# Optimization experiments

Measured on AMD Instinct MI355X. Metric: run time of the kernel, lower is better.

## Reference

```python
import jax, jax.numpy as jnp
import numpy as np

SEQ_LEN = 1024
BATCH = 256
HIDDEN = 100
OUT = 1

L_FILTER = [-0.0106, 0.0329, 0.0308, -0.187, -0.028, 0.6309, 0.7148, 0.2304]
H_FILTER = [-0.2304, 0.7148, -0.6309, -0.028, 0.187, 0.0308, -0.0329, -0.0106]


def _create_W(P, is_l, rng):
    filt = L_FILTER if is_l else H_FILTER
    eps = np.min(np.abs(filt))
    W = rng.standard_normal((P, P)) * 0.1 * eps
    for i in range(P):
        for k, j in enumerate(range(i, min(i + len(filt), P))):
            W[i, j] = filt[k]
    return jnp.asarray(W, dtype=jnp.float32)


def setup_inputs() -> dict:
    key = jax.random.key(0)
    ks = jax.random.split(key, 16)
    rng = np.random.default_rng(0)
    T, H = SEQ_LEN, HIDDEN
    s = 1.0 / np.sqrt(H)

    def lstm_params(k):
        k1, k2, k3 = jax.random.split(k, 3)
        Wih = jax.random.uniform(k1, (4 * H, 1), jnp.float32, -s, s)
        Whh = jax.random.uniform(k2, (4 * H, H), jnp.float32, -s, s)
        b = jax.random.uniform(k3, (4 * H,), jnp.float32, -s, s)
        return Wih, Whh, b

    Wih1, Whh1, b1 = lstm_params(ks[0])
    Wih2, Whh2, b2 = lstm_params(ks[1])
    Wih3, Whh3, b3 = lstm_params(ks[2])
    return {
        "x": jax.random.normal(ks[3], (BATCH, T, 1), jnp.float32),
        "W1H": _create_W(T, False, rng),
        "b1H": jax.random.uniform(ks[4], (T,), jnp.float32, -1 / np.sqrt(T), 1 / np.sqrt(T)),
        "W1L": _create_W(T, True, rng),
        "b1L": jax.random.uniform(ks[5], (T,), jnp.float32, -1 / np.sqrt(T), 1 / np.sqrt(T)),
        "W2H": _create_W(T // 2, False, rng),
        "b2H": jax.random.uniform(ks[6], (T // 2,), jnp.float32, -1 / np.sqrt(T // 2), 1 / np.sqrt(T // 2)),
        "W2L": _create_W(T // 2, True, rng),
        "b2L": jax.random.uniform(ks[7], (T // 2,), jnp.float32, -1 / np.sqrt(T // 2), 1 / np.sqrt(T // 2)),
        "Wih1": Wih1, "Whh1": Whh1, "b1": b1,
        "Wih2": Wih2, "Whh2": Whh2, "b2": b2,
        "Wih3": Wih3, "Whh3": Whh3, "b3": b3,
        "Wout": jax.random.uniform(ks[8], (OUT, H), jnp.float32, -s, s),
        "bout": jax.random.uniform(ks[9], (OUT,), jnp.float32, -s, s),
    }


def _avgpool2(x):  # [B, L] -> [B, L//2], AvgPool1d(kernel=2, stride=2)
    B, L = x.shape
    return x.reshape(B, L // 2, 2).mean(-1)


def _lstm(x, Wih, Whh, b):
    # x: [B, T, 1]; torch LSTM gate order i, f, g, o; h0 = c0 = 0
    H = Whh.shape[1]
    gx = jnp.einsum('bti,gi->btg', x, Wih) + b  # [B, T, 4H]

    def step(carry, g):
        h, c = carry
        z = g + h @ Whh.T
        i, f, gg, o = jnp.split(z, 4, axis=-1)
        c = jax.nn.sigmoid(f) * c + jax.nn.sigmoid(i) * jnp.tanh(gg)
        h = jax.nn.sigmoid(o) * jnp.tanh(c)
        return (h, c), h

    B = x.shape[0]
    h0 = jnp.zeros((B, H), x.dtype)
    _, hs = jax.lax.scan(step, (h0, h0), jnp.swapaxes(gx, 0, 1))
    return jnp.swapaxes(hs, 0, 1)  # [B, T, H]


def reference(x, W1H, b1H, W1L, b1L, W2H, b2H, W2L, b2L,
              Wih1, Whh1, b1, Wih2, Whh2, b2, Wih3, Whh3, b3, Wout, bout):
    inp = x[:, :, -1]  # [B, T]
    ah1 = jax.nn.sigmoid(inp @ W1H.T + b1H)
    al1 = jax.nn.sigmoid(inp @ W1L.T + b1L)
    xh1 = _avgpool2(ah1)  # [B, T/2]
    xl1 = _avgpool2(al1)  # [B, T/2]
    ah2 = jax.nn.sigmoid(xl1 @ W2H.T + b2H)
    al2 = jax.nn.sigmoid(xl1 @ W2L.T + b2L)
    xh2 = _avgpool2(ah2)  # [B, T/4]
    xl2 = _avgpool2(al2)  # [B, T/4]
    s1 = _lstm(xh1[..., None], Wih1, Whh1, b1)
    s2 = _lstm(xh2[..., None], Wih2, Whh2, b2)
    s3 = _lstm(xl2[..., None], Wih3, Whh3, b3)
    cat = jnp.concatenate([s1, s2, s3], axis=1)  # [B, T, H]
    out = cat @ Wout.T + bout  # [B, T, OUT]
    return out[:, -1, :]
```

## Files before the change

### kernel.cpp

```cpp
#include <hip/hip_runtime.h>
#include <math.h>

typedef __bf16 bf16x8 __attribute__((ext_vector_type(8)));
typedef _Float16 f16x8 __attribute__((ext_vector_type(8)));
typedef _Float16 f16x4 __attribute__((ext_vector_type(4)));
typedef float f32x4 __attribute__((ext_vector_type(4)));

#define LOG2E 1.44269504f
#define TWOL2E 2.88539008f

__device__ __forceinline__ unsigned short f2bf(float f) {
  unsigned int u = __builtin_bit_cast(unsigned int, f);
  u += 0x7fffu + ((u >> 16) & 1u);
  return (unsigned short)(u >> 16);
}
__device__ __forceinline__ unsigned int pack2bf(float a, float b) {
  return (unsigned int)f2bf(a) | ((unsigned int)f2bf(b) << 16);
}

#define GK_PAD2 72
template <int WFP32, int XFP32, int DO_PREP, int NXB>
__global__ __launch_bounds__(256) void gemm_mfma_sig_pool(
    const void* __restrict__ Wv, const float* __restrict__ bias,
    const void* __restrict__ Xv, void* __restrict__ Y,
    int K, int Np, int out_bf16,
    const float* __restrict__ Whh, const float* __restrict__ b3,
    _Float16* __restrict__ P) {
  if (DO_PREP && blockIdx.x == NXB) {
    const int base = blockIdx.y * 256 + threadIdx.x;
    for (int idx = base; idx < 400 * 16; idx += 4096) {
      const int row = idx >> 4, ch = idx & 15;
      const int hid = row >> 2, gate = row & 3;
      const int src = gate * 100 + hid;
      const float s = (gate == 2) ? TWOL2E : LOG2E;
      f16x8 v;
#pragma unroll
      for (int j = 0; j < 8; j++) {
        const int k = ch * 8 + j;
        float f = 0.f;
        if (k < 100) f = Whh[(size_t)src * 100 + k] * s;
        v[j] = (_Float16)f;
      }
      *(f16x8*)&P[(size_t)row * 128 + ch * 8] = v;
    }
    return;
  }

  __shared__ unsigned short Wt[64][GK_PAD2];
  __shared__ unsigned short Xt[16][GK_PAD2];
  const int tid = threadIdx.x;
  const int i_base = blockIdx.x * 64;
  const int b_base = blockIdx.y * 16;
  const int srow = tid >> 2, sseg = tid & 3;
  const int xr = tid >> 4, xs = tid & 15;
  const int wv = tid >> 6, lane = tid & 63;
  const int L15 = lane & 15, q = lane >> 4;

  const float* Wf = (const float*)Wv;
  const float* Xf = (const float*)Xv;
  const unsigned short* Wh = (const unsigned short*)Wv;
  const unsigned short* Xh = (const unsigned short*)Xv;

  float4 wf[2][4];
  uint4 wh[2][2];
  float4 xf[2];
  uint2 xh2[2];

#define LOADW(S, KO)                                                          \
  do {                                                                        \
    if (WFP32) {                                                              \
      _Pragma("unroll") for (int j = 0; j < 4; j++)                           \
          wf[S][j] = *(const float4*)&Wf[(size_t)(i_base + srow) * K + (KO) + \
                                         sseg * 16 + 4 * j];                  \
    } else {                                                                  \
      _Pragma("unroll") for (int j = 0; j < 2; j++)                           \
          wh[S][j] = *(const uint4*)&Wh[(size_t)(i_base + srow) * K + (KO) +  \
                                        sseg * 16 + 8 * j];                   \
    }                                                                         \
  } while (0)

#define LOADX(S, KO)                                                          \
  do {                                                                        \
    if (XFP32) {                                                              \
      xf[S] = *(const float4*)&Xf[(size_t)(b_base + xr) * K + (KO) + xs * 4]; \
    } else {                                                                  \
      xh2[S] = *(const uint2*)&Xh[(size_t)(b_base + xr) * K + (KO) + xs * 4]; \
    }                                                                         \
  } while (0)

#define STAGEW(S)                                                             \
  do {                                                                        \
    if (WFP32) {                                                              \
      uint4 p0 = {pack2bf(wf[S][0].x, wf[S][0].y),                            \
                  pack2bf(wf[S][0].z, wf[S][0].w),                            \
                  pack2bf(wf[S][1].x, wf[S][1].y),                            \
                  pack2bf(wf[S][1].z, wf[S][1].w)};                           \
      uint4 p1 = {pack2bf(wf[S][2].x, wf[S][2].y),                            \
                  pack2bf(wf[S][2].z, wf[S][2].w),                            \
                  pack2bf(wf[S][3].x, wf[S][3].y),                            \
                  pack2bf(wf[S][3].z, wf[S][3].w)};                           \
      *(uint4*)&Wt[srow][sseg * 16] = p0;                                     \
      *(uint4*)&Wt[srow][sseg * 16 + 8] = p1;                                 \
    } else {                                                                  \
      *(uint4*)&Wt[srow][sseg * 16] = wh[S][0];                               \
      *(uint4*)&Wt[srow][sseg * 16 + 8] = wh[S][1];                           \
    }                                                                         \
  } while (0)

#define STAGEX(S)                                                             \
  do {                                                                        \
    if (XFP32) {                                                              \
      uint2 p = {pack2bf(xf[S].x, xf[S].y), pack2bf(xf[S].z, xf[S].w)};       \
      *(uint2*)&Xt[xr][xs * 4] = p;                                           \
    } else {                                                                  \
      *(uint2*)&Xt[xr][xs * 4] = xh2[S];                                      \
    }                                                                         \
  } while (0)

#define DOMFMA                                                                \
  do {                                                                        \
    _Pragma("unroll") for (int kt = 0; kt < 2; kt++) {                        \
      bf16x8 a = *(const bf16x8*)&Wt[wv * 16 + L15][kt * 32 + q * 8];         \
      bf16x8 b = *(const bf16x8*)&Xt[L15][kt * 32 + q * 8];                   \
      acc = __builtin_amdgcn_mfma_f32_16x16x32_bf16(a, b, acc, 0, 0, 0);      \
    }                                                                         \
  } while (0)

  f32x4 acc = {};
  LOADW(0, 0);
  LOADX(0, 0);
  for (int k0 = 0; k0 < K; k0 += 128) {
    LOADW(1, k0 + 64);
    LOADX(1, k0 + 64);
    STAGEW(0);
    STAGEX(0);
    __syncthreads();
    DOMFMA;
    __syncthreads();
    if (k0 + 128 < K) {
      LOADW(0, k0 + 128);
      LOADX(0, k0 + 128);
    }
    STAGEW(1);
    STAGEX(1);
    __syncthreads();
    DOMFMA;
    __syncthreads();
  }
#undef LOADW
#undef LOADX
#undef STAGEW
#undef STAGEX
#undef DOMFMA

  {
    const int nrow = i_base + 16 * wv + q * 4;
    const float bi0 = bias[nrow], bi1 = bias[nrow + 1];
    const float bi2 = bias[nrow + 2], bi3 = bias[nrow + 3];
    const int b = b_base + L15;
    const float a0 = __builtin_amdgcn_rcpf(1.f + __expf(-(acc[0] + bi0)));
    const float a1 = __builtin_amdgcn_rcpf(1.f + __expf(-(acc[1] + bi1)));
    const float a2 = __builtin_amdgcn_rcpf(1.f + __expf(-(acc[2] + bi2)));
    const float a3 = __builtin_amdgcn_rcpf(1.f + __expf(-(acc[3] + bi3)));
    const float p0 = 0.5f * (a0 + a1), p1 = 0.5f * (a2 + a3);
    const int pidx = nrow >> 1;
    if (out_bf16) {
      *(unsigned int*)&((unsigned short*)Y)[(size_t)b * Np + pidx] = pack2bf(p0, p1);
    } else {
      *(float2*)&((float*)Y)[(size_t)b * Np + pidx] = make_float2(p0, p1);
    }
  }
}

#define TSTEPS 256

__device__ __forceinline__ float qb0(float x) {
  return __builtin_bit_cast(float, __builtin_amdgcn_mov_dpp(__builtin_bit_cast(int, x), 0x00, 0xf, 0xf, true));
}
__device__ __forceinline__ float qb1(float x) {
  return __builtin_bit_cast(float, __builtin_amdgcn_mov_dpp(__builtin_bit_cast(int, x), 0x55, 0xf, 0xf, true));
}
__device__ __forceinline__ float qb2(float x) {
  return __builtin_bit_cast(float, __builtin_amdgcn_mov_dpp(__builtin_bit_cast(int, x), 0xAA, 0xf, 0xf, true));
}
__device__ __forceinline__ float qb3(float x) {
  return __builtin_bit_cast(float, __builtin_amdgcn_mov_dpp(__builtin_bit_cast(int, x), 0xFF, 0xf, 0xf, true));
}

__global__ __launch_bounds__(512, 2) void lstm_mfma(
    const float* __restrict__ X, const _Float16* __restrict__ P,
    const float* __restrict__ Whh, const float* __restrict__ Wih,
    const float* __restrict__ b3, const float* __restrict__ Wout,
    const float* __restrict__ bout, float* __restrict__ out) {
  const int bat = blockIdx.x;
  const int t = threadIdx.x;
  const int w = t >> 6, lane = t & 63;
  const int quad = lane >> 4, c = lane & 15;
  const int TB = (w == 7) ? 21 : w * 3;
  const int NT = (w == 7) ? 4 : 3;

  __shared__ __align__(16) _Float16 hbuf[2][128];
  __shared__ float xrow[TSTEPS];
  __shared__ float red[128];

  for (int i = t; i < TSTEPS; i += 512) xrow[i] = X[(size_t)bat * TSTEPS + i];
  if (t < 128) { hbuf[0][t] = (_Float16)0.f; hbuf[1][t] = (_Float16)0.f; }

#define LDA(J, KT) const f16x8 A##J##KT = \
    *(const f16x8*)&P[(size_t)((TB + J) * 16 + c) * 128 + (KT) * 32 + quad * 8];
  LDA(0,0) LDA(0,1) LDA(0,2)
  LDA(1,0) LDA(1,1) LDA(1,2)
  LDA(2,0) LDA(2,1) LDA(2,2)
  LDA(3,0) LDA(3,1) LDA(3,2)
#undef LDA

  const bool act = (c < 4 * NT);
  const int J = c >> 2, g = c & 3;
  const int myhid = 4 * (TB + (act ? J : 0)) + quad;
  const int grow = g * 100 + myhid;
  const float sc = (g == 2) ? TWOL2E : LOG2E;
  const float u_ = Wih[grow] * sc;
  const float bz = b3[grow] * sc;
  const float4 wt0 = *(const float4*)&Whh[(size_t)grow * 100 + 96];
  const float4 wt = make_float4(wt0.x * sc, wt0.y * sc, wt0.z * sc, wt0.w * sc);
  const float mm = (g == 2) ? 2.f : 1.f;
  const float dd = (g == 2) ? -1.f : 0.f;
  float cst = 0.f;
  __syncthreads();

#define SIG2(zz) __builtin_amdgcn_rcpf(1.f + __builtin_amdgcn_exp2f(-(zz)))
#define STEPB(HC, HN, XT)                                                      \
  {                                                                            \
    const _Float16* hc = (HC);                                                 \
    const f16x8 B0 = *(const f16x8*)&hc[0 * 32 + quad * 8];                    \
    const f16x8 B1 = *(const f16x8*)&hc[1 * 32 + quad * 8];                    \
    const f16x8 B2 = *(const f16x8*)&hc[2 * 32 + quad * 8];                    \
    const f16x4 ht = *(const f16x4*)&hc[96];   \
    f32x4 z0 = {0.f,0.f,0.f,0.f}, z1 = z0, z2 = z0, z3 = z0;                   \
    { f32x4 za = z0, zb = z0;                                                  \
      za = __builtin_amdgcn_mfma_f32_16x16x32_f16(A00, B0, za, 0, 0, 0);       \
      zb = __builtin_amdgcn_mfma_f32_16x16x32_f16(A01, B1, zb, 0, 0, 0);       \
      za = __builtin_amdgcn_mfma_f32_16x16x32_f16(A02, B2, za, 0, 0, 0);       \
      z0 = za + zb; }                                                          \
    { f32x4 za = {0.f,0.f,0.f,0.f}, zb = za;                                   \
      za = __builtin_amdgcn_mfma_f32_16x16x32_f16(A10, B0, za, 0, 0, 0);       \
      zb = __builtin_amdgcn_mfma_f32_16x16x32_f16(A11, B1, zb, 0, 0, 0);       \
      za = __builtin_amdgcn_mfma_f32_16x16x32_f16(A12, B2, za, 0, 0, 0);       \
      z1 = za + zb; }                                                          \
    { f32x4 za = {0.f,0.f,0.f,0.f}, zb = za;                                   \
      za = __builtin_amdgcn_mfma_f32_16x16x32_f16(A20, B0, za, 0, 0, 0);       \
      zb = __builtin_amdgcn_mfma_f32_16x16x32_f16(A21, B1, zb, 0, 0, 0);       \
      za = __builtin_amdgcn_mfma_f32_16x16x32_f16(A22, B2, za, 0, 0, 0);       \
      z2 = za + zb; }                                                          \
    if (w == 7) {                                                              \
      f32x4 za = {0.f,0.f,0.f,0.f}, zb = za;                                   \
      za = __builtin_amdgcn_mfma_f32_16x16x32_f16(A30, B0, za, 0, 0, 0);       \
      zb = __builtin_amdgcn_mfma_f32_16x16x32_f16(A31, B1, zb, 0, 0, 0);       \
      za = __builtin_amdgcn_mfma_f32_16x16x32_f16(A32, B2, za, 0, 0, 0);       \
      z3 = za + zb; }                                                          \
    if (act) {                                                                 \
      const f32x4 zt = (J == 0) ? z0 : (J == 1) ? z1 : (J == 2) ? z2 : z3;     \
      const float zsel = (g == 0) ? zt[0] : (g == 1) ? zt[1]                   \
                       : (g == 2) ? zt[2] : zt[3];                             \
      const float t0 = fmaf(wt.x, (float)ht[0], fmaf(wt.y, (float)ht[1], bz)); \
      const float t1 = fmaf(wt.z, (float)ht[2],                                \
                            fmaf(wt.w, (float)ht[3], u_ * (XT)));              \
      const float zs = (zsel + t0) + t1;                                       \
      const float a = mm * SIG2(zs) + dd;                                      \
      const float ai = qb0(a), af = qb1(a), ag = qb2(a), ao = qb3(a);          \
      cst = fmaf(af, cst, ai * ag);                                            \
      const float th = 2.f * SIG2(TWOL2E * cst) - 1.f;                         \
      if (g == 0) (HN)[myhid] = (_Float16)(ao * th);                           \
    }                                                                          \
    __syncthreads();                                                           \
  }

  for (int step = 0; step < TSTEPS; step += 2) {
    STEPB(hbuf[0], hbuf[1], xrow[step]);
    STEPB(hbuf[1], hbuf[0], xrow[step + 1]);
  }
#undef STEPB
#undef SIG2

  if (t < 128) {
    float a = 0.f;
    if (t < 100) a = (float)hbuf[0][t] * Wout[t];
    red[t] = a;
  }
  __syncthreads();
  if (t == 0) {
    float s = 0.f;
#pragma unroll
    for (int k = 0; k < 128; k++) s += red[k];
    out[bat] = s + bout[0];
  }
}

extern "C" void kernel_launch(void* const* d_in, const int* in_sizes, int n_in,
                              void* d_out, int out_size, void* d_ws, size_t ws_size,
                              hipStream_t stream) {
  const float* x    = (const float*)d_in[0];
  const float* W1L  = (const float*)d_in[3];
  const float* b1L  = (const float*)d_in[4];
  const float* W2L  = (const float*)d_in[7];
  const float* b2L  = (const float*)d_in[8];
  const float* Wih3 = (const float*)d_in[15];
  const float* Whh3 = (const float*)d_in[16];
  const float* b3   = (const float*)d_in[17];
  const float* Wout = (const float*)d_in[18];
  const float* bout = (const float*)d_in[19];
  float* out = (float*)d_out;

  unsigned short* xl1b = (unsigned short*)d_ws;
  float* xl2 = (float*)(xl1b + (size_t)256 * 512);
  _Float16* P = (_Float16*)(xl2 + (size_t)256 * 256);

  gemm_mfma_sig_pool<1, 1, 0, 16><<<dim3(16, 16), 256, 0, stream>>>(
      W1L, b1L, x, xl1b, 1024, 512, 1, nullptr, nullptr, nullptr);
  gemm_mfma_sig_pool<1, 0, 1, 8><<<dim3(9, 16), 256, 0, stream>>>(
      W2L, b2L, xl1b, xl2, 512, 256, 0, Whh3, b3, P);
  lstm_mfma<<<256, 512, 0, stream>>>(xl2, P, Whh3, Wih3, b3, Wout, bout, out);
}
```

Before: 231.1 us.

## Halve LSTM block to four waves, each computing up to seven gate tiles

The recurrent LSTM kernel now uses 256 threads (4 wavefronts) per batch row instead of 512 (8 wavefronts). Each wave handles 6 or 7 16-row gate tiles and two hidden-unit slots per lane, which doubles the per-lane cell state and the activation work. The aim is to make the per-step __syncthreads barrier cheaper by having fewer waves join it. The cost is a longer serial MFMA and activation chain per wave, and more registers held for the A fragments.

Result: slower. 291.3 us (+26.1%).

```diff
diff --git a/kernel.cpp b/kernel.cpp
--- a/kernel.cpp
+++ b/kernel.cpp
@@ -187,7 +187,7 @@
   return __builtin_bit_cast(float, __builtin_amdgcn_mov_dpp(__builtin_bit_cast(int, x), 0xFF, 0xf, 0xf, true));
 }
 
-__global__ __launch_bounds__(512, 2) void lstm_mfma(
+__global__ __launch_bounds__(256, 1) void lstm_mfma4(
     const float* __restrict__ X, const _Float16* __restrict__ P,
     const float* __restrict__ Whh, const float* __restrict__ Wih,
     const float* __restrict__ b3, const float* __restrict__ Wout,
@@ -196,14 +196,14 @@
   const int t = threadIdx.x;
   const int w = t >> 6, lane = t & 63;
   const int quad = lane >> 4, c = lane & 15;
-  const int TB = (w == 7) ? 21 : w * 3;
-  const int NT = (w == 7) ? 4 : 3;
+  const int TB = 6 * w;
+  const int NT = (w == 3) ? 7 : 6;
 
   __shared__ __align__(16) _Float16 hbuf[2][128];
   __shared__ float xrow[TSTEPS];
   __shared__ float red[128];
 
-  for (int i = t; i < TSTEPS; i += 512) xrow[i] = X[(size_t)bat * TSTEPS + i];
+  for (int i = t; i < TSTEPS; i += 256) xrow[i] = X[(size_t)bat * TSTEPS + i];
   if (t < 128) { hbuf[0][t] = (_Float16)0.f; hbuf[1][t] = (_Float16)0.f; }
 
 #define LDA(J, KT) const f16x8 A##J##KT = \
@@ -212,65 +212,76 @@
   LDA(1,0) LDA(1,1) LDA(1,2)
   LDA(2,0) LDA(2,1) LDA(2,2)
   LDA(3,0) LDA(3,1) LDA(3,2)
+  LDA(4,0) LDA(4,1) LDA(4,2)
+  LDA(5,0) LDA(5,1) LDA(5,2)
+  LDA(6,0) LDA(6,1) LDA(6,2)
 #undef LDA
 
-  const bool act = (c < 4 * NT);
-  const int J = c >> 2, g = c & 3;
-  const int myhid = 4 * (TB + (act ? J : 0)) + quad;
-  const int grow = g * 100 + myhid;
+  const int g = c & 3, Jq = c >> 2;
+  const bool act2 = (Jq < NT - 4);
+  const int hid1 = 4 * (TB + Jq) + quad;
+  const int hid2 = 4 * (TB + 4 + Jq) + quad;
+  const int grow1 = g * 100 + hid1;
+  const int grow2 = g * 100 + hid2;
   const float sc = (g == 2) ? TWOL2E : LOG2E;
-  const float u_ = Wih[grow] * sc;
-  const float bz = b3[grow] * sc;
-  const float4 wt0 = *(const float4*)&Whh[(size_t)grow * 100 + 96];
-  const float4 wt = make_float4(wt0.x * sc, wt0.y * sc, wt0.z * sc, wt0.w * sc);
+  const float u1 = Wih[grow1] * sc, bz1 = b3[grow1] * sc;
+  const float u2 = Wih[grow2] * sc, bz2 = b3[grow2] * sc;
+  const float4 wt1r = *(const float4*)&Whh[(size_t)grow1 * 100 + 96];
+  const float4 wt2r = *(const float4*)&Whh[(size_t)grow2 * 100 + 96];
+  const float4 wt1 = make_float4(wt1r.x * sc, wt1r.y * sc, wt1r.z * sc, wt1r.w * sc);
+  const float4 wt2 = make_float4(wt2r.x * sc, wt2r.y * sc, wt2r.z * sc, wt2r.w * sc);
   const float mm = (g == 2) ? 2.f : 1.f;
   const float dd = (g == 2) ? -1.f : 0.f;
-  float cst = 0.f;
+  float cst1 = 0.f, cst2 = 0.f;
   __syncthreads();
 
 #define SIG2(zz) __builtin_amdgcn_rcpf(1.f + __builtin_amdgcn_exp2f(-(zz)))
+#define ZTILE(ZN, J)                                                           \
+    f32x4 ZN;                                                                  \
+    { f32x4 za = {0.f,0.f,0.f,0.f}, zb = za;                                   \
+      za = __builtin_amdgcn_mfma_f32_16x16x32_f16(A##J##0, B0, za, 0, 0, 0);   \
+      zb = __builtin_amdgcn_mfma_f32_16x16x32_f16(A##J##1, B1, zb, 0, 0, 0);   \
+      za = __builtin_amdgcn_mfma_f32_16x16x32_f16(A##J##2, B2, za, 0, 0, 0);   \
+      ZN = za + zb; }
+
 #define STEPB(HC, HN, XT)                                                      \
   {                                                                            \
     const _Float16* hc = (HC);                                                 \
     const f16x8 B0 = *(const f16x8*)&hc[0 * 32 + quad * 8];                    \
     const f16x8 B1 = *(const f16x8*)&hc[1 * 32 + quad * 8];                    \
     const f16x8 B2 = *(const f16x8*)&hc[2 * 32 + quad * 8];                    \
-    const f16x4 ht = *(const f16x4*)&hc[96];   \
-    f32x4 z0 = {0.f,0.f,0.f,0.f}, z1 = z0, z2 = z0, z3 = z0;                   \
-    { f32x4 za = z0, zb = z0;                                                  \
-      za = __builtin_amdgcn_mfma_f32_16x16x32_f16(A00, B0, za, 0, 0, 0);       \
-      zb = __builtin_amdgcn_mfma_f32_16x16x32_f16(A01, B1, zb, 0, 0, 0);       \
-      za = __builtin_amdgcn_mfma_f32_16x16x32_f16(A02, B2, za, 0, 0, 0);       \
-      z0 = za + zb; }                                                          \
-    { f32x4 za = {0.f,0.f,0.f,0.f}, zb = za;                                   \
-      za = __builtin_amdgcn_mfma_f32_16x16x32_f16(A10, B0, za, 0, 0, 0);       \
-      zb = __builtin_amdgcn_mfma_f32_16x16x32_f16(A11, B1, zb, 0, 0, 0);       \
-      za = __builtin_amdgcn_mfma_f32_16x16x32_f16(A12, B2, za, 0, 0, 0);       \
-      z1 = za + zb; }                                                          \
-    { f32x4 za = {0.f,0.f,0.f,0.f}, zb = za;                                   \
-      za = __builtin_amdgcn_mfma_f32_16x16x32_f16(A20, B0, za, 0, 0, 0);       \
-      zb = __builtin_amdgcn_mfma_f32_16x16x32_f16(A21, B1, zb, 0, 0, 0);       \
-      za = __builtin_amdgcn_mfma_f32_16x16x32_f16(A22, B2, za, 0, 0, 0);       \
-      z2 = za + zb; }                                                          \
-    if (w == 7) {                                                              \
-      f32x4 za = {0.f,0.f,0.f,0.f}, zb = za;                                   \
-      za = __builtin_amdgcn_mfma_f32_16x16x32_f16(A30, B0, za, 0, 0, 0);       \
-      zb = __builtin_amdgcn_mfma_f32_16x16x32_f16(A31, B1, zb, 0, 0, 0);       \
-      za = __builtin_amdgcn_mfma_f32_16x16x32_f16(A32, B2, za, 0, 0, 0);       \
-      z3 = za + zb; }                                                          \
-    if (act) {                                                                 \
-      const f32x4 zt = (J == 0) ? z0 : (J == 1) ? z1 : (J == 2) ? z2 : z3;     \
-      const float zsel = (g == 0) ? zt[0] : (g == 1) ? zt[1]                   \
-                       : (g == 2) ? zt[2] : zt[3];                             \
-      const float t0 = fmaf(wt.x, (float)ht[0], fmaf(wt.y, (float)ht[1], bz)); \
-      const float t1 = fmaf(wt.z, (float)ht[2],                                \
-                            fmaf(wt.w, (float)ht[3], u_ * (XT)));              \
+    const f16x4 ht = *(const f16x4*)&hc[96];                                   \
+    ZTILE(z0, 0) ZTILE(z1, 1) ZTILE(z2, 2) ZTILE(z3, 3)                        \
+    ZTILE(z4, 4) ZTILE(z5, 5) ZTILE(z6, 6)                                     \
+                                                       \
+    {                                                                          \
+      const f32x4 zA = (Jq == 0) ? z0 : (Jq == 1) ? z1 : (Jq == 2) ? z2 : z3;  \
+      const float zsel = (g == 0) ? zA[0] : (g == 1) ? zA[1]                   \
+                       : (g == 2) ? zA[2] : zA[3];                             \
+      const float t0 = fmaf(wt1.x, (float)ht[0], fmaf(wt1.y, (float)ht[1], bz1)); \
+      const float t1 = fmaf(wt1.z, (float)ht[2],                               \
+                            fmaf(wt1.w, (float)ht[3], u1 * (XT)));             \
       const float zs = (zsel + t0) + t1;                                       \
       const float a = mm * SIG2(zs) + dd;                                      \
       const float ai = qb0(a), af = qb1(a), ag = qb2(a), ao = qb3(a);          \
-      cst = fmaf(af, cst, ai * ag);                                            \
-      const float th = 2.f * SIG2(TWOL2E * cst) - 1.f;                         \
-      if (g == 0) (HN)[myhid] = (_Float16)(ao * th);                           \
+      cst1 = fmaf(af, cst1, ai * ag);                                          \
+      const float th = 2.f * SIG2(TWOL2E * cst1) - 1.f;                        \
+      if (g == 0) (HN)[hid1] = (_Float16)(ao * th);                            \
+    }                                                                          \
+                                                   \
+    if (act2) {                                                                \
+      const f32x4 zB = (Jq == 0) ? z4 : (Jq == 1) ? z5 : z6;                   \
+      const float zsel = (g == 0) ? zB[0] : (g == 1) ? zB[1]                   \
+                       : (g == 2) ? zB[2] : zB[3];                             \
+      const float t0 = fmaf(wt2.x, (float)ht[0], fmaf(wt2.y, (float)ht[1], bz2)); \
+      const float t1 = fmaf(wt2.z, (float)ht[2],                               \
+                            fmaf(wt2.w, (float)ht[3], u2 * (XT)));             \
+      const float zs = (zsel + t0) + t1;                                       \
+      const float a = mm * SIG2(zs) + dd;                                      \
+      const float ai = qb0(a), af = qb1(a), ag = qb2(a), ao = qb3(a);          \
+      cst2 = fmaf(af, cst2, ai * ag);                                          \
+      const float th = 2.f * SIG2(TWOL2E * cst2) - 1.f;                        \
+      if (g == 0) (HN)[hid2] = (_Float16)(ao * th);                            \
     }                                                                          \
     __syncthreads();                                                           \
   }
@@ -280,6 +291,7 @@
     STEPB(hbuf[1], hbuf[0], xrow[step + 1]);
   }
 #undef STEPB
+#undef ZTILE
 #undef SIG2
 
   if (t < 128) {
@@ -319,5 +331,5 @@
       W1L, b1L, x, xl1b, 1024, 512, 1, nullptr, nullptr, nullptr);
   gemm_mfma_sig_pool<1, 0, 1, 8><<<dim3(9, 16), 256, 0, stream>>>(
       W2L, b2L, xl1b, xl2, 512, 256, 0, Whh3, b3, P);
-  lstm_mfma<<<256, 512, 0, stream>>>(xl2, P, Whh3, Wih3, b3, Wout, bout, out);
-}
+  lstm_mfma4<<<256, 256, 0, stream>>>(xl2, P, Whh3, Wih3, b3, Wout, bout, out);
+}
```
